# Kernel optimization log

Hardware: AMD Instinct MI355X
Metric: run time of the kernel (lower is better)

The kernel has to match this reference:

```python
import jax, jax.numpy as jnp
import numpy as np

B, S, T = 16, 256, 2048
V, D, H, L, FF, NM = 3000, 512, 8, 6, 2048, 80
DH = D // H


def _make_pe(max_len=5000, d=D):
    pos = np.arange(max_len, dtype=np.float32)[:, None]
    div = np.exp(np.arange(0, d, 2, dtype=np.float32) * (-np.log(10000.0) / d))
    pe = np.zeros((max_len, d), dtype=np.float32)
    pe[:, 0::2] = np.sin(pos * div)
    pe[:, 1::2] = np.cos(pos * div)
    return jnp.asarray(pe[None])  # [1, max_len, D]


def setup_inputs() -> dict:
    key = jax.random.key(0)
    ks = jax.random.split(key, 24)
    f = jnp.float32
    n = lambda k, sh, s=0.02: jax.random.normal(k, sh, f) * s
    return {
        'text_ids': jax.random.randint(ks[0], (B, S), 0, V),
        'text_lengths': jax.random.randint(ks[1], (B,), S // 2, S + 1),
        'mel_targets': jax.random.normal(ks[2], (B, NM, T), f),
        'emb': n(ks[3], (V, D), 0.05),
        'pe': _make_pe(),
        'Wqkv': n(ks[4], (L, D, 3 * D)), 'bqkv': jnp.zeros((L, 3 * D), f),
        'Wo': n(ks[5], (L, D, D)), 'bo': jnp.zeros((L, D), f),
        'ln1_s': jnp.ones((L, D), f), 'ln1_b': jnp.zeros((L, D), f),
        'ln2_s': jnp.ones((L, D), f), 'ln2_b': jnp.zeros((L, D), f),
        'W1': n(ks[6], (L, D, FF)), 'b1': jnp.zeros((L, FF), f),
        'W2': n(ks[7], (L, FF, D)), 'b2': jnp.zeros((L, D), f),
        'mel_W1': n(ks[8], (D, FF)), 'mel_b1': jnp.zeros((FF,), f),
        'mel_W2': n(ks[9], (FF, NM)), 'mel_b2': jnp.zeros((NM,), f),
        'dur_W1': n(ks[10], (D, 256)), 'dur_b1': jnp.zeros((256,), f),
        'dur_W2': n(ks[11], (256, 1)), 'dur_b2': jnp.zeros((1,), f),
    }


def _layer_norm(x, s, b, eps=1e-5):
    m = jnp.mean(x, -1, keepdims=True)
    v = jnp.mean(jnp.square(x - m), -1, keepdims=True)
    return (x - m) * jax.lax.rsqrt(v + eps) * s + b


def _length_regulate(enc, durations, target_len):
    # enc [B,S,D], durations [B,S] -> [B,target_len,D]
    dur = jnp.maximum(jnp.round(durations).astype(jnp.int32), 1)
    cum = jnp.cumsum(dur, axis=1)                              # [B,S] inclusive
    pos = jnp.arange(target_len)                               # [T]
    idx = jnp.sum(pos[None, None, :] >= cum[:, :, None], axis=1)  # [B,T]
    idx = jnp.minimum(idx, enc.shape[1] - 1)
    valid = pos[None, :] < cum[:, -1:]                         # [B,T]
    out = jnp.take_along_axis(enc, idx[..., None], axis=1)
    return out * valid[..., None].astype(enc.dtype)


def reference(text_ids, text_lengths, mel_targets, emb, pe, Wqkv, bqkv, Wo, bo,
              ln1_s, ln1_b, ln2_s, ln2_b, W1, b1, W2, b2,
              mel_W1, mel_b1, mel_W2, mel_b2, dur_W1, dur_b1, dur_W2, dur_b2):
    x = emb[text_ids] + pe[:, :S]                              # [B,S,D]
    pad = jnp.arange(S)[None, :] >= text_lengths[:, None]      # True = padded key
    bias = jnp.where(pad, -1e9, 0.0)[:, None, None, :]         # [B,1,1,S]
    scale = 1.0 / jnp.sqrt(jnp.float32(DH))
    for l in range(L):
        qkv = x @ Wqkv[l] + bqkv[l]
        q, k, v = jnp.split(qkv, 3, axis=-1)
        q = q.reshape(B, S, H, DH).transpose(0, 2, 1, 3)
        k = k.reshape(B, S, H, DH).transpose(0, 2, 1, 3)
        v = v.reshape(B, S, H, DH).transpose(0, 2, 1, 3)
        scores = jnp.einsum('bhqd,bhkd->bhqk', q, k) * scale + bias
        attn = jax.nn.softmax(scores, axis=-1)
        o = jnp.einsum('bhqk,bhkd->bhqd', attn, v)
        o = o.transpose(0, 2, 1, 3).reshape(B, S, D) @ Wo[l] + bo[l]
        x = _layer_norm(x + o, ln1_s[l], ln1_b[l])              # post-LN (torch default)
        ff = jax.nn.relu(x @ W1[l] + b1[l]) @ W2[l] + b2[l]
        x = _layer_norm(x + ff, ln2_s[l], ln2_b[l])
    enc = x
    dur_h = jax.nn.relu(enc @ dur_W1 + dur_b1)
    durations = jax.nn.softplus((dur_h @ dur_W2 + dur_b2).squeeze(-1))  # [B,S]
    target_len = mel_targets.shape[2]
    expanded = _length_regulate(enc, durations, target_len)    # [B,T,D]
    mel = jax.nn.relu(expanded @ mel_W1 + mel_b1) @ mel_W2 + mel_b2
    mel = mel.transpose(0, 2, 1)                               # [B,NM,T]
    return mel, durations, enc
```

## Files before the change

### kernel.cpp

```cpp
#include <hip/hip_runtime.h>
#include <math.h>

#define B_ 16
#define S_ 256
#define T_ 2048
#define D_ 512
#define H_ 8
#define L_ 6
#define FF_ 2048
#define NM_ 80
#define M_ 4096

typedef float floatx4 __attribute__((ext_vector_type(4)));
typedef __bf16 bf16x8 __attribute__((ext_vector_type(8)));

__device__ __forceinline__ float bf2f(unsigned u) {
    return __uint_as_float((u & 0xffffu) << 16);
}
__device__ __forceinline__ unsigned short f2bf(float f) {
    unsigned u = __float_as_uint(f);
    unsigned r = u + 0x7fffu + ((u >> 16) & 1u);
    return (unsigned short)(r >> 16);
}
__device__ __forceinline__ void gload_lds16(const void* g, void* l) {
    __builtin_amdgcn_global_load_lds(
        (const __attribute__((address_space(1))) void*)g,
        (__attribute__((address_space(3))) void*)l, 16, 0, 0);
}

__global__ __launch_bounds__(256) void transpose_bf16(
    const float* __restrict__ src, unsigned short* __restrict__ dst,
    int K, int N)
{
    __shared__ float tile[32][33];
    const int k0 = blockIdx.y * 32, n0 = blockIdx.x * 32;
    src += (size_t)blockIdx.z * K * N;
    dst += (size_t)blockIdx.z * K * N;
    const int tx = threadIdx.x, ty = threadIdx.y;
#pragma unroll
    for (int i = 0; i < 32; i += 8)
        tile[ty + i][tx] = src[(size_t)(k0 + ty + i) * N + n0 + tx];
    __syncthreads();
#pragma unroll
    for (int i = 0; i < 32; i += 8)
        dst[(size_t)(n0 + ty + i) * K + k0 + tx] = f2bf(tile[tx][ty + i]);
}

__global__ __launch_bounds__(256) void transpose_pad_bf16(
    const float* __restrict__ src, unsigned short* __restrict__ dst,
    int K, int Ns)
{
    __shared__ float tile[32][33];
    const int k0 = blockIdx.y * 32, n0 = blockIdx.x * 32;
    const int tx = threadIdx.x, ty = threadIdx.y;
#pragma unroll
    for (int i = 0; i < 32; i += 8) {
        int n = n0 + tx;
        tile[ty + i][tx] = (n < Ns) ? src[(size_t)(k0 + ty + i) * Ns + n] : 0.f;
    }
    __syncthreads();
#pragma unroll
    for (int i = 0; i < 32; i += 8)
        dst[(size_t)(n0 + ty + i) * K + k0 + tx] = f2bf(tile[tx][ty + i]);
}

__global__ __launch_bounds__(128) void embed_bf16(
    const int* __restrict__ ids, const float* __restrict__ emb,
    const float* __restrict__ pe, unsigned short* __restrict__ x)
{
    const int r = blockIdx.x;
    const int c = threadIdx.x * 4;
    const int id = ids[r];
    const int s = r & (S_ - 1);
    float4 e = *(const float4*)(emb + (size_t)id * D_ + c);
    float4 p = *(const float4*)(pe + (size_t)s * D_ + c);
    ushort4 o;
    o.x = f2bf(e.x + p.x); o.y = f2bf(e.y + p.y);
    o.z = f2bf(e.z + p.z); o.w = f2bf(e.w + p.w);
    *(ushort4*)(x + (size_t)r * D_ + c) = o;
}

template<int BM, int BN>
__global__ __launch_bounds__(256) void gemm2(
    const unsigned short* __restrict__ A, const unsigned short* __restrict__ Bt,
    const float* __restrict__ bias, unsigned short* __restrict__ Cb,
    float* __restrict__ Cpart, int N, int klen, int act)
{
    constexpr int NSUB_A = BM / 8;
    constexpr int NSUB_B = BN / 8;
    constexpr int NSUB = NSUB_A + NSUB_B;
    constexpr int NL = NSUB / 4;
    constexpr int BUFSZ = NSUB * 1024;
    constexpr int AOFF = NSUB_A * 1024;
    constexpr int WM = BM / 32, WN = BN / 32;
    __shared__ __attribute__((aligned(16))) char smem[2 * BUFSZ];

    const int tid = threadIdx.x;
    const int wave = tid >> 6, lane = tid & 63;
    const int lm = lane & 15, quad = lane >> 4;
    const int wm = wave >> 1, wn = wave & 1;
    const int m0 = blockIdx.y * BM;
    const int n0 = blockIdx.x * BN;
    const int Kfull = klen * gridDim.z;
    const int kb = blockIdx.z * klen;

    floatx4 acc[WM][WN];
#pragma unroll
    for (int i = 0; i < WM; i++)
#pragma unroll
        for (int j = 0; j < WN; j++) acc[i][j] = (floatx4){0.f, 0.f, 0.f, 0.f};

    const unsigned short* ga[NL];
    int loff[NL];
#pragma unroll
    for (int j = 0; j < NL; j++) {
        int sid = wave * NL + j;
        if (sid < NSUB_A) {
            int mi = sid >> 1, ki = sid & 1;
            ga[j] = A + (size_t)(m0 + mi * 16 + lm) * Kfull + kb + ki * 32 + quad * 8;
            loff[j] = sid * 1024;
        } else {
            int t = sid - NSUB_A;
            int ni = t >> 1, ki = t & 1;
            ga[j] = Bt + (size_t)(n0 + ni * 16 + lm) * Kfull + kb + ki * 32 + quad * 8;
            loff[j] = AOFF + t * 1024;
        }
    }

#pragma unroll
    for (int j = 0; j < NL; j++) gload_lds16(ga[j], smem + loff[j]);

    for (int kt = 0; kt < klen; kt += 64) {
        char* sc = smem + ((kt >> 6) & 1) * BUFSZ;
        if (kt + 64 < klen) {
            char* sn = smem + (((kt >> 6) + 1) & 1) * BUFSZ;
#pragma unroll
            for (int j = 0; j < NL; j++) gload_lds16(ga[j] + kt + 64, sn + loff[j]);
            __builtin_amdgcn_s_waitcnt(0x0F70 | NL);
        } else {
            __builtin_amdgcn_s_waitcnt(0x0F70);
        }
        asm volatile("" ::: "memory");
        __builtin_amdgcn_s_barrier();
        asm volatile("" ::: "memory");

#pragma unroll
        for (int ki = 0; ki < 2; ki++) {
            bf16x8 af[WM], bfr[WN];
#pragma unroll
            for (int i = 0; i < WM; i++)
                af[i] = *(const bf16x8*)(sc + ((((wm * WM + i) * 2 + ki) << 10) + (lane << 4)));
#pragma unroll
            for (int j = 0; j < WN; j++)
                bfr[j] = *(const bf16x8*)(sc + AOFF + ((((wn * WN + j) * 2 + ki) << 10) + (lane << 4)));
#pragma unroll
            for (int i = 0; i < WM; i++)
#pragma unroll
                for (int j = 0; j < WN; j++)
                    acc[i][j] = __builtin_amdgcn_mfma_f32_16x16x32_bf16(
                        af[i], bfr[j], acc[i][j], 0, 0, 0);
        }
        asm volatile("" ::: "memory");
        __builtin_amdgcn_s_barrier();
        asm volatile("" ::: "memory");
    }

    if (gridDim.z == 1) {
#pragma unroll
        for (int mi = 0; mi < WM; mi++) {
            const int rb = m0 + wm * (WM * 16) + mi * 16 + quad * 4;
#pragma unroll
            for (int nj = 0; nj < WN; nj++) {
                const int col = n0 + wn * (WN * 16) + nj * 16 + lm;
                const float bv = bias[col];
#pragma unroll
                for (int r = 0; r < 4; r++) {
                    float o = acc[mi][nj][r] + bv;
                    if (act) o = fmaxf(o, 0.f);
                    Cb[(size_t)(rb + r) * N + col] = f2bf(o);
                }
            }
        }
    } else {
        float* Cp = Cpart + (size_t)blockIdx.z * gridDim.y * BM * N;
#pragma unroll
        for (int mi = 0; mi < WM; mi++) {
            const int rb = m0 + wm * (WM * 16) + mi * 16 + quad * 4;
#pragma unroll
            for (int nj = 0; nj < WN; nj++) {
                const int col = n0 + wn * (WN * 16) + nj * 16 + lm;
#pragma unroll
                for (int r = 0; r < 4; r++)
                    Cp[(size_t)(rb + r) * N + col] = acc[mi][nj][r];
            }
        }
    }
}

__global__ __launch_bounds__(256) void transpose_v(
    const unsigned short* __restrict__ qkv, unsigned short* __restrict__ vt)
{
    __shared__ unsigned short tile[64][74];
    const int tid = threadIdx.x;
    const int bh = blockIdx.y;
    const int b = bh >> 3, h = bh & 7;
    const int s0 = blockIdx.x * 64;
    const int ty = tid >> 3, tx = tid & 7;
#pragma unroll
    for (int i = 0; i < 64; i += 32) {
        uint4 v = *(const uint4*)(qkv + (size_t)(b * 256 + s0 + ty + i) * 1536
                                  + 1024 + h * 64 + tx * 8);
        unsigned short* dstp = &tile[ty + i][tx * 8];
        const unsigned short* sp = (const unsigned short*)&v;
#pragma unroll
        for (int j = 0; j < 8; j++) dstp[j] = sp[j];
    }
    __syncthreads();
#pragma unroll
    for (int i = 0; i < 64; i += 32) {
        int d = ty + i;
        unsigned short tmp[8];
#pragma unroll
        for (int j = 0; j < 8; j++) tmp[j] = tile[tx * 8 + j][d];
        *(uint4*)(vt + (size_t)(bh * 64 + d) * 256 + s0 + tx * 8) = *(uint4*)tmp;
    }
}

__global__ __launch_bounds__(256) void attn_fused(
    const unsigned short* __restrict__ qkv, const unsigned short* __restrict__ vt,
    const int* __restrict__ lens, unsigned short* __restrict__ o)
{
    __shared__ __attribute__((aligned(16))) char smem[32768];
    const int tid = threadIdx.x;
    const int wave = tid >> 6, lane = tid & 63;
    const int lm = lane & 15, quad = lane >> 4;
    const int qt = blockIdx.x;
    const int bh = blockIdx.y;
    const int b = bh >> 3, h = bh & 7;
    const int len = lens[b];
    const unsigned short* Qb = qkv + ((size_t)b * 256 + qt * 64) * 1536 + h * 64;
    const unsigned short* Kb = qkv + (size_t)b * 256 * 1536 + 512 + h * 64;
    const unsigned short* Vt = vt + (size_t)bh * 64 * 256;
    const int rbase = wave * 16;

#pragma unroll
    for (int j = 0; j < 8; j++) {
        int sid = wave * 8 + j;
        int nf = sid >> 1, kf = sid & 1;
        gload_lds16(Kb + (size_t)(nf * 16 + lm) * 1536 + kf * 32 + quad * 8,
                    smem + sid * 1024);
    }
    bf16x8 aq[2];
#pragma unroll
    for (int kf = 0; kf < 2; kf++)
        aq[kf] = *(const bf16x8*)(Qb + (size_t)(rbase + lm) * 1536 + kf * 32 + quad * 8);
    __syncthreads();

    floatx4 accS[16];
#pragma unroll
    for (int nf = 0; nf < 16; nf++) accS[nf] = (floatx4){0.f, 0.f, 0.f, 0.f};

#pragma unroll
    for (int nf = 0; nf < 16; nf++) {
        bf16x8 bk0 = *(const bf16x8*)(smem + (nf * 2 + 0) * 1024 + lane * 16);
        bf16x8 bk1 = *(const bf16x8*)(smem + (nf * 2 + 1) * 1024 + lane * 16);
        accS[nf] = __builtin_amdgcn_mfma_f32_16x16x32_bf16(aq[0], bk0, accS[nf], 0, 0, 0);
        accS[nf] = __builtin_amdgcn_mfma_f32_16x16x32_bf16(aq[1], bk1, accS[nf], 0, 0, 0);
    }

    float lrow[4];
    const float scale = 0.125f;
#pragma unroll
    for (int r = 0; r < 4; r++) {
        float mx = -1e30f;
#pragma unroll
        for (int nf = 0; nf < 16; nf++) {
            float s = accS[nf][r] * scale + ((nf * 16 + lm >= len) ? -1e9f : 0.f);
            accS[nf][r] = s;
            mx = fmaxf(mx, s);
        }
#pragma unroll
        for (int off = 1; off < 16; off <<= 1) mx = fmaxf(mx, __shfl_xor(mx, off, 64));
        float sum = 0.f;
#pragma unroll
        for (int nf = 0; nf < 16; nf++) {
            float e = __expf(accS[nf][r] - mx);
            accS[nf][r] = e;
            sum += e;
        }
#pragma unroll
        for (int off = 1; off < 16; off <<= 1) sum += __shfl_xor(sum, off, 64);
        lrow[r] = sum;
    }

    floatx4 accO[4];
#pragma unroll
    for (int nj = 0; nj < 4; nj++) accO[nj] = (floatx4){0.f, 0.f, 0.f, 0.f};

    unsigned short* sP = (unsigned short*)smem;
#pragma unroll
    for (int half = 0; half < 2; half++) {
        __syncthreads();
#pragma unroll
        for (int nf2 = 0; nf2 < 8; nf2++) {
            int nf = half * 8 + nf2;
            int row = rbase + quad * 4;
            int col = nf2 * 16 + lm;
#pragma unroll
            for (int r = 0; r < 4; r++)
                sP[(row + r) * 136 + col] = f2bf(accS[nf][r]);
        }
        __syncthreads();
#pragma unroll
        for (int ks2 = 0; ks2 < 4; ks2++) {
            bf16x8 ap = *(const bf16x8*)(sP + (rbase + lm) * 136 + ks2 * 32 + quad * 8);
            int ks = half * 4 + ks2;
#pragma unroll
            for (int nj = 0; nj < 4; nj++) {
                bf16x8 bv = *(const bf16x8*)(Vt + (size_t)(nj * 16 + lm) * 256
                                             + ks * 32 + quad * 8);
                accO[nj] = __builtin_amdgcn_mfma_f32_16x16x32_bf16(ap, bv, accO[nj], 0, 0, 0);
            }
        }
    }

    float inv[4];
#pragma unroll
    for (int r = 0; r < 4; r++) inv[r] = 1.f / lrow[r];
    const int grow = b * 256 + qt * 64 + rbase + quad * 4;
#pragma unroll
    for (int nj = 0; nj < 4; nj++) {
        const int gcol = h * 64 + nj * 16 + lm;
#pragma unroll
        for (int r = 0; r < 4; r++)
            o[(size_t)(grow + r) * 512 + gcol] = f2bf(accO[nj][r] * inv[r]);
    }
}

__global__ __launch_bounds__(128) void add_ln_bf16(
    unsigned short* __restrict__ x, const unsigned short* __restrict__ y,
    const float* __restrict__ s, const float* __restrict__ bb)
{
    __shared__ float red[2];
    const int row = blockIdx.x;
    const int tid = threadIdx.x;
    const int c = tid * 4;
    ushort4 xv = *(const ushort4*)(x + (size_t)row * D_ + c);
    ushort4 yv = *(const ushort4*)(y + (size_t)row * D_ + c);
    float h[4];
    h[0] = bf2f(xv.x) + bf2f(yv.x);
    h[1] = bf2f(xv.y) + bf2f(yv.y);
    h[2] = bf2f(xv.z) + bf2f(yv.z);
    h[3] = bf2f(xv.w) + bf2f(yv.w);

    float sum = h[0] + h[1] + h[2] + h[3];
#pragma unroll
    for (int off = 32; off >= 1; off >>= 1) sum += __shfl_xor(sum, off, 64);
    if ((tid & 63) == 0) red[tid >> 6] = sum;
    __syncthreads();
    float mean = (red[0] + red[1]) * (1.f / 512.f);
    __syncthreads();

    float d[4];
    d[0] = h[0] - mean; d[1] = h[1] - mean; d[2] = h[2] - mean; d[3] = h[3] - mean;
    float sq = d[0] * d[0] + d[1] * d[1] + d[2] * d[2] + d[3] * d[3];
#pragma unroll
    for (int off = 32; off >= 1; off >>= 1) sq += __shfl_xor(sq, off, 64);
    if ((tid & 63) == 0) red[tid >> 6] = sq;
    __syncthreads();
    float var = (red[0] + red[1]) * (1.f / 512.f);
    float rs = rsqrtf(var + 1e-5f);

    float4 sv = *(const float4*)(s + c);
    float4 bv = *(const float4*)(bb + c);
    ushort4 ov;
    ov.x = f2bf(d[0] * rs * sv.x + bv.x);
    ov.y = f2bf(d[1] * rs * sv.y + bv.y);
    ov.z = f2bf(d[2] * rs * sv.z + bv.z);
    ov.w = f2bf(d[3] * rs * sv.w + bv.w);
    *(ushort4*)(x + (size_t)row * D_ + c) = ov;
}

__global__ __launch_bounds__(128) void add_ln_part(
    unsigned short* __restrict__ x, const float* __restrict__ p0,
    const float* __restrict__ p1, const float* __restrict__ bias,
    const float* __restrict__ s, const float* __restrict__ bb,
    float* __restrict__ enc_opt)
{
    __shared__ float red[2];
    const int row = blockIdx.x;
    const int tid = threadIdx.x;
    const int c = tid * 4;
    ushort4 xv = *(const ushort4*)(x + (size_t)row * D_ + c);
    float4 a = *(const float4*)(p0 + (size_t)row * D_ + c);
    float4 bq = *(const float4*)(p1 + (size_t)row * D_ + c);
    float4 bi = *(const float4*)(bias + c);
    float h[4];
    h[0] = bf2f(xv.x) + a.x + bq.x + bi.x;
    h[1] = bf2f(xv.y) + a.y + bq.y + bi.y;
    h[2] = bf2f(xv.z) + a.z + bq.z + bi.z;
    h[3] = bf2f(xv.w) + a.w + bq.w + bi.w;

    float sum = h[0] + h[1] + h[2] + h[3];
#pragma unroll
    for (int off = 32; off >= 1; off >>= 1) sum += __shfl_xor(sum, off, 64);
    if ((tid & 63) == 0) red[tid >> 6] = sum;
    __syncthreads();
    float mean = (red[0] + red[1]) * (1.f / 512.f);
    __syncthreads();

    float d[4];
    d[0] = h[0] - mean; d[1] = h[1] - mean; d[2] = h[2] - mean; d[3] = h[3] - mean;
    float sq = d[0] * d[0] + d[1] * d[1] + d[2] * d[2] + d[3] * d[3];
#pragma unroll
    for (int off = 32; off >= 1; off >>= 1) sq += __shfl_xor(sq, off, 64);
    if ((tid & 63) == 0) red[tid >> 6] = sq;
    __syncthreads();
    float var = (red[0] + red[1]) * (1.f / 512.f);
    float rs = rsqrtf(var + 1e-5f);

    float4 sv = *(const float4*)(s + c);
    float4 bv = *(const float4*)(bb + c);
    float o[4];
    o[0] = d[0] * rs * sv.x + bv.x;
    o[1] = d[1] * rs * sv.y + bv.y;
    o[2] = d[2] * rs * sv.z + bv.z;
    o[3] = d[3] * rs * sv.w + bv.w;
    ushort4 ov;
    ov.x = f2bf(o[0]); ov.y = f2bf(o[1]); ov.z = f2bf(o[2]); ov.w = f2bf(o[3]);
    *(ushort4*)(x + (size_t)row * D_ + c) = ov;
    if (enc_opt) {
        float4 e; e.x = o[0]; e.y = o[1]; e.z = o[2]; e.w = o[3];
        *(float4*)(enc_opt + (size_t)row * D_ + c) = e;
    }
}

__global__ __launch_bounds__(256) void dur_head2(
    const float* __restrict__ p0, const float* __restrict__ p1,
    const float* __restrict__ b1, const float* __restrict__ w2,
    const float* __restrict__ b2, float* __restrict__ durout)
{
    const int tid = threadIdx.x;
    const int w = tid >> 6, lane = tid & 63;
    const int r = blockIdx.x * 4 + w;
    float4 a = *(const float4*)(p0 + (size_t)r * 256 + lane * 4);
    float4 bq = *(const float4*)(p1 + (size_t)r * 256 + lane * 4);
    float4 bi = *(const float4*)(b1 + lane * 4);
    float4 wv = *(const float4*)(w2 + lane * 4);
    float h0 = fmaxf(a.x + bq.x + bi.x, 0.f);
    float h1 = fmaxf(a.y + bq.y + bi.y, 0.f);
    float h2 = fmaxf(a.z + bq.z + bi.z, 0.f);
    float h3 = fmaxf(a.w + bq.w + bi.w, 0.f);
    float p = h0 * wv.x + h1 * wv.y + h2 * wv.z + h3 * wv.w;
#pragma unroll
    for (int off = 32; off >= 1; off >>= 1) p += __shfl_xor(p, off, 64);
    if (lane == 0) {
        float v = p + b2[0];
        durout[r] = (v > 20.f) ? v : log1pf(expf(v));
    }
}

__global__ __launch_bounds__(256) void dur_cumsum(
    const float* __restrict__ dur, int* __restrict__ cum)
{
    __shared__ int sc[256];
    const int b = blockIdx.x, s = threadIdx.x;
    int d = (int)rintf(dur[b * 256 + s]);
    if (d < 1) d = 1;
    sc[s] = d;
    __syncthreads();
    for (int off = 1; off < 256; off <<= 1) {
        int v = sc[s];
        int add = (s >= off) ? sc[s - off] : 0;
        __syncthreads();
        sc[s] = v + add;
        __syncthreads();
    }
    cum[b * 256 + s] = sc[s];
}

__global__ __launch_bounds__(256) void mel_c0(
    const float* __restrict__ b1, const float* __restrict__ W2,
    const float* __restrict__ b2, float* __restrict__ c0)
{
    __shared__ float red[4];
    const int c = blockIdx.x;
    const int tid = threadIdx.x;
    float p = 0.f;
    for (int f = tid; f < 2048; f += 256)
        p += fmaxf(b1[f], 0.f) * W2[(size_t)f * 80 + c];
#pragma unroll
    for (int off = 32; off >= 1; off >>= 1) p += __shfl_xor(p, off, 64);
    if ((tid & 63) == 0) red[tid >> 6] = p;
    __syncthreads();
    if (tid == 0) c0[c] = red[0] + red[1] + red[2] + red[3] + b2[c];
}

__global__ __launch_bounds__(256) void mel_gather2(
    const float* __restrict__ mp, const float* __restrict__ b2,
    const float* __restrict__ c0, const int* __restrict__ cum,
    float* __restrict__ mel_out)
{
    __shared__ float rows[256 * 40];
    __shared__ int sc[256];
    __shared__ float s0[40];
    const int tid = threadIdx.x;
    const int b = blockIdx.z;
    const int cc0 = blockIdx.y * 40;
    sc[tid] = cum[b * 256 + tid];
    if (tid < 40) s0[tid] = c0[cc0 + tid];
    const size_t plane = (size_t)M_ * 128;
    for (int idx = tid; idx < 256 * 40; idx += 256) {
        int r = idx / 40, c = idx - r * 40;
        size_t base = ((size_t)b * 256 + r) * 128 + cc0 + c;
        rows[idx] = mp[base] + mp[plane + base] + mp[2 * plane + base]
                  + mp[3 * plane + base] + b2[cc0 + c];
    }
    __syncthreads();
    const int total = sc[255];
    const int t = blockIdx.x * 256 + tid;
    int lo = 0, hi = 256;
    while (lo < hi) {
        int mid = (lo + hi) >> 1;
        if (sc[mid] <= t) lo = mid + 1; else hi = mid;
    }
    int row = lo < 255 ? lo : 255;
    const bool valid = t < total;
    const float* src = valid ? &rows[row * 40] : s0;
    for (int cc = 0; cc < 40; cc++)
        mel_out[((size_t)b * 80 + cc0 + cc) * T_ + t] = src[cc];
}

extern "C" void kernel_launch(void* const* d_in, const int* in_sizes, int n_in,
                              void* d_out, int out_size, void* d_ws, size_t ws_size,
                              hipStream_t stream)
{
    const int*   text_ids     = (const int*)d_in[0];
    const int*   text_lengths = (const int*)d_in[1];
    const float* emb   = (const float*)d_in[3];
    const float* pe    = (const float*)d_in[4];
    const float* Wqkv  = (const float*)d_in[5];
    const float* bqkv  = (const float*)d_in[6];
    const float* Wo    = (const float*)d_in[7];
    const float* bo    = (const float*)d_in[8];
    const float* ln1_s = (const float*)d_in[9];
    const float* ln1_b = (const float*)d_in[10];
    const float* ln2_s = (const float*)d_in[11];
    const float* ln2_b = (const float*)d_in[12];
    const float* W1    = (const float*)d_in[13];
    const float* b1    = (const float*)d_in[14];
    const float* W2    = (const float*)d_in[15];
    const float* b2    = (const float*)d_in[16];
    const float* mel_W1 = (const float*)d_in[17];
    const float* mel_b1 = (const float*)d_in[18];
    const float* mel_W2 = (const float*)d_in[19];
    const float* mel_b2 = (const float*)d_in[20];
    const float* dur_W1 = (const float*)d_in[21];
    const float* dur_b1 = (const float*)d_in[22];
    const float* dur_W2 = (const float*)d_in[23];
    const float* dur_b2 = (const float*)d_in[24];

    float* out = (float*)d_out;
    float* mel_out = out;
    float* dur_out = out + (size_t)B_ * NM_ * T_;
    float* enc_out = dur_out + (size_t)B_ * S_;

    typedef unsigned short u16;
    char* w = (char*)d_ws;
    u16* Wqkv_t  = (u16*)w;                   w += (size_t)L_ * 1536 * 512 * 2;
    u16* Wo_t    = (u16*)w;                   w += (size_t)L_ * 512 * 512 * 2;
    u16* W1_t    = (u16*)w;                   w += (size_t)L_ * 2048 * 512 * 2;
    u16* W2_t    = (u16*)w;                   w += (size_t)L_ * 512 * 2048 * 2;
    u16* melW1_t = (u16*)w;                   w += (size_t)2048 * 512 * 2;
    u16* melW2_t = (u16*)w;                   w += (size_t)128 * 2048 * 2;
    u16* durW1_t = (u16*)w;                   w += (size_t)256 * 512 * 2;
    u16* x_bf    = (u16*)w;                   w += (size_t)M_ * 512 * 2;
    u16* qkv_bf  = (u16*)w;                   w += (size_t)M_ * 1536 * 2;
    u16* ao_bf   = (u16*)w;                   w += (size_t)M_ * 512 * 2;
    u16* y_bf    = (u16*)w;                   w += (size_t)M_ * 512 * 2;
    char* big    = w;                         w += (size_t)16777216;
    float* c0    = (float*)w;                 w += 512;
    int*   cum   = (int*)w;                   w += (size_t)M_ * 4;

    u16* ffh     = (u16*)big;
    u16* melh    = (u16*)big;
    u16* vt      = (u16*)(big + 12582912);

    float* part2 = (float*)qkv_bf;
    float* dpart = (float*)qkv_bf;
    float* mpart = (float*)(qkv_bf + (size_t)M_ * 512);

    transpose_bf16<<<dim3(48, 16, 6), dim3(32, 8), 0, stream>>>(Wqkv, Wqkv_t, 512, 1536);
    transpose_bf16<<<dim3(16, 16, 6), dim3(32, 8), 0, stream>>>(Wo, Wo_t, 512, 512);
    transpose_bf16<<<dim3(64, 16, 6), dim3(32, 8), 0, stream>>>(W1, W1_t, 512, 2048);
    transpose_bf16<<<dim3(16, 64, 6), dim3(32, 8), 0, stream>>>(W2, W2_t, 2048, 512);
    transpose_bf16<<<dim3(64, 16, 1), dim3(32, 8), 0, stream>>>(mel_W1, melW1_t, 512, 2048);
    transpose_pad_bf16<<<dim3(4, 64), dim3(32, 8), 0, stream>>>(mel_W2, melW2_t, 2048, 80);
    transpose_bf16<<<dim3(8, 16, 1), dim3(32, 8), 0, stream>>>(dur_W1, durW1_t, 512, 256);

    embed_bf16<<<M_, 128, 0, stream>>>(text_ids, emb, pe, x_bf);

    for (int l = 0; l < L_; l++) {
        gemm2<64, 128><<<dim3(12, 64), 256, 0, stream>>>(
            x_bf, Wqkv_t + (size_t)l * 1536 * 512, bqkv + (size_t)l * 1536,
            qkv_bf, nullptr, 1536, 512, 0);
        transpose_v<<<dim3(4, 128), 256, 0, stream>>>(qkv_bf, vt);
        attn_fused<<<dim3(4, 128), 256, 0, stream>>>(qkv_bf, vt, text_lengths, ao_bf);
        gemm2<64, 64><<<dim3(8, 64), 256, 0, stream>>>(
            ao_bf, Wo_t + (size_t)l * 512 * 512, bo + (size_t)l * 512,
            y_bf, nullptr, 512, 512, 0);
        add_ln_bf16<<<M_, 128, 0, stream>>>(
            x_bf, y_bf, ln1_s + (size_t)l * D_, ln1_b + (size_t)l * D_);
        gemm2<64, 128><<<dim3(16, 64), 256, 0, stream>>>(
            x_bf, W1_t + (size_t)l * 2048 * 512, b1 + (size_t)l * 2048,
            ffh, nullptr, 2048, 512, 1);
        gemm2<64, 64><<<dim3(8, 64, 2), 256, 0, stream>>>(
            ffh, W2_t + (size_t)l * 512 * 2048, nullptr,
            nullptr, part2, 512, 1024, 0);
        add_ln_part<<<M_, 128, 0, stream>>>(
            x_bf, part2, part2 + (size_t)M_ * 512, b2 + (size_t)l * 512,
            ln2_s + (size_t)l * D_, ln2_b + (size_t)l * D_,
            (l == L_ - 1) ? enc_out : nullptr);
    }

    gemm2<64, 64><<<dim3(4, 64, 2), 256, 0, stream>>>(
        x_bf, durW1_t, nullptr, nullptr, dpart, 256, 256, 0);
    dur_head2<<<M_ / 4, 256, 0, stream>>>(
        dpart, dpart + (size_t)M_ * 256, dur_b1, dur_W2, dur_b2, dur_out);
    dur_cumsum<<<B_, 256, 0, stream>>>(dur_out, cum);

    gemm2<64, 128><<<dim3(16, 64), 256, 0, stream>>>(
        x_bf, melW1_t, mel_b1, melh, nullptr, 2048, 512, 1);
    gemm2<64, 128><<<dim3(1, 64, 4), 256, 0, stream>>>(
        melh, melW2_t, nullptr, nullptr, mpart, 128, 512, 0);
    mel_c0<<<NM_, 256, 0, stream>>>(mel_b1, mel_W2, mel_b2, c0);
    mel_gather2<<<dim3(T_ / 256, 2, B_), 256, 0, stream>>>(mpart, mel_b2, c0, cum, mel_out);
}
```

Baseline: 993.8 us.

## Fuse V transpose into QKV GEMM epilogue and enlarge GEMM and attention tiles

The QKV GEMM now writes the V block transposed through shared memory straight into the vt buffer, which removes the separate transpose_v kernel and its extra read of qkv. Every GEMM moves to 128-row M tiles, and the attention kernel handles 128 queries per block with two MFMA row groups per wave. Together these cut launches and redundant K loads, but they halve the block count and raise register pressure.

```diff
diff --git a/kernel.cpp b/kernel.cpp
--- a/kernel.cpp
+++ b/kernel.cpp
@@ -84,7 +84,8 @@
 __global__ __launch_bounds__(256) void gemm2(
     const unsigned short* __restrict__ A, const unsigned short* __restrict__ Bt,
     const float* __restrict__ bias, unsigned short* __restrict__ Cb,
-    float* __restrict__ Cpart, int N, int klen, int act)
+    float* __restrict__ Cpart, unsigned short* __restrict__ vtp,
+    int N, int klen, int act)
 {
     constexpr int NSUB_A = BM / 8;
     constexpr int NSUB_B = BN / 8;
@@ -165,6 +166,40 @@
         asm volatile("" ::: "memory");
     }
 
+    if constexpr (BM == 128 && BN == 128) {
+        if (vtp != nullptr && n0 >= 1024) {
+            unsigned short* sT = (unsigned short*)smem;
+#pragma unroll
+            for (int mi = 0; mi < WM; mi++) {
+                const int rl = wm * 64 + mi * 16 + quad * 4;
+#pragma unroll
+                for (int nj = 0; nj < WN; nj++) {
+                    const int cl = wn * 64 + nj * 16 + lm;
+                    const float bv = bias[n0 + cl];
+                    ushort4 t4;
+                    t4.x = f2bf(acc[mi][nj][0] + bv);
+                    t4.y = f2bf(acc[mi][nj][1] + bv);
+                    t4.z = f2bf(acc[mi][nj][2] + bv);
+                    t4.w = f2bf(acc[mi][nj][3] + bv);
+                    *(ushort4*)(sT + cl * 136 + rl) = t4;
+                }
+            }
+            __syncthreads();
+            const int b = m0 >> 8;
+            const int s0 = m0 & 255;
+            const int h0 = (n0 - 1024) >> 6;
+#pragma unroll
+            for (int i = 0; i < 8; i++) {
+                int idx = i * 256 + tid;
+                int d = idx >> 4, c = idx & 15;
+                uint4 v = *(const uint4*)(sT + d * 136 + c * 8);
+                int bh = b * 8 + h0 + (d >> 6);
+                *(uint4*)(vtp + ((size_t)bh * 64 + (d & 63)) * 256 + s0 + c * 8) = v;
+            }
+            return;
+        }
+    }
+
     if (gridDim.z == 1) {
 #pragma unroll
         for (int mi = 0; mi < WM; mi++) {
@@ -197,40 +232,11 @@
     }
 }
 
-__global__ __launch_bounds__(256) void transpose_v(
-    const unsigned short* __restrict__ qkv, unsigned short* __restrict__ vt)
-{
-    __shared__ unsigned short tile[64][74];
-    const int tid = threadIdx.x;
-    const int bh = blockIdx.y;
-    const int b = bh >> 3, h = bh & 7;
-    const int s0 = blockIdx.x * 64;
-    const int ty = tid >> 3, tx = tid & 7;
-#pragma unroll
-    for (int i = 0; i < 64; i += 32) {
-        uint4 v = *(const uint4*)(qkv + (size_t)(b * 256 + s0 + ty + i) * 1536
-                                  + 1024 + h * 64 + tx * 8);
-        unsigned short* dstp = &tile[ty + i][tx * 8];
-        const unsigned short* sp = (const unsigned short*)&v;
-#pragma unroll
-        for (int j = 0; j < 8; j++) dstp[j] = sp[j];
-    }
-    __syncthreads();
-#pragma unroll
-    for (int i = 0; i < 64; i += 32) {
-        int d = ty + i;
-        unsigned short tmp[8];
-#pragma unroll
-        for (int j = 0; j < 8; j++) tmp[j] = tile[tx * 8 + j][d];
-        *(uint4*)(vt + (size_t)(bh * 64 + d) * 256 + s0 + tx * 8) = *(uint4*)tmp;
-    }
-}
-
 __global__ __launch_bounds__(256) void attn_fused(
     const unsigned short* __restrict__ qkv, const unsigned short* __restrict__ vt,
     const int* __restrict__ lens, unsigned short* __restrict__ o)
 {
-    __shared__ __attribute__((aligned(16))) char smem[32768];
+    __shared__ __attribute__((aligned(16))) char smem[34816];
     const int tid = threadIdx.x;
     const int wave = tid >> 6, lane = tid & 63;
     const int lm = lane & 15, quad = lane >> 4;
@@ -238,10 +244,9 @@
     const int bh = blockIdx.y;
     const int b = bh >> 3, h = bh & 7;
     const int len = lens[b];
-    const unsigned short* Qb = qkv + ((size_t)b * 256 + qt * 64) * 1536 + h * 64;
+    const unsigned short* Qb = qkv + ((size_t)b * 256 + qt * 128) * 1536 + h * 64;
     const unsigned short* Kb = qkv + (size_t)b * 256 * 1536 + 512 + h * 64;
     const unsigned short* Vt = vt + (size_t)bh * 64 * 256;
-    const int rbase = wave * 16;
 
 #pragma unroll
     for (int j = 0; j < 8; j++) {
@@ -250,90 +255,112 @@
         gload_lds16(Kb + (size_t)(nf * 16 + lm) * 1536 + kf * 32 + quad * 8,
                     smem + sid * 1024);
     }
-    bf16x8 aq[2];
-#pragma unroll
-    for (int kf = 0; kf < 2; kf++)
-        aq[kf] = *(const bf16x8*)(Qb + (size_t)(rbase + lm) * 1536 + kf * 32 + quad * 8);
-    __syncthreads();
-
-    floatx4 accS[16];
-#pragma unroll
-    for (int nf = 0; nf < 16; nf++) accS[nf] = (floatx4){0.f, 0.f, 0.f, 0.f};
+    bf16x8 aq[2][2];
+#pragma unroll
+    for (int mi = 0; mi < 2; mi++)
+#pragma unroll
+        for (int kf = 0; kf < 2; kf++)
+            aq[mi][kf] = *(const bf16x8*)(Qb + (size_t)(wave * 32 + mi * 16 + lm) * 1536
+                                          + kf * 32 + quad * 8);
+    __syncthreads();
+
+    floatx4 accS[2][16];
+#pragma unroll
+    for (int mi = 0; mi < 2; mi++)
+#pragma unroll
+        for (int nf = 0; nf < 16; nf++) accS[mi][nf] = (floatx4){0.f, 0.f, 0.f, 0.f};
 
 #pragma unroll
     for (int nf = 0; nf < 16; nf++) {
         bf16x8 bk0 = *(const bf16x8*)(smem + (nf * 2 + 0) * 1024 + lane * 16);
         bf16x8 bk1 = *(const bf16x8*)(smem + (nf * 2 + 1) * 1024 + lane * 16);
-        accS[nf] = __builtin_amdgcn_mfma_f32_16x16x32_bf16(aq[0], bk0, accS[nf], 0, 0, 0);
-        accS[nf] = __builtin_amdgcn_mfma_f32_16x16x32_bf16(aq[1], bk1, accS[nf], 0, 0, 0);
-    }
-
-    float lrow[4];
+        accS[0][nf] = __builtin_amdgcn_mfma_f32_16x16x32_bf16(aq[0][0], bk0, accS[0][nf], 0, 0, 0);
+        accS[0][nf] = __builtin_amdgcn_mfma_f32_16x16x32_bf16(aq[0][1], bk1, accS[0][nf], 0, 0, 0);
+        accS[1][nf] = __builtin_amdgcn_mfma_f32_16x16x32_bf16(aq[1][0], bk0, accS[1][nf], 0, 0, 0);
+        accS[1][nf] = __builtin_amdgcn_mfma_f32_16x16x32_bf16(aq[1][1], bk1, accS[1][nf], 0, 0, 0);
+    }
+
+    float lrow[2][4];
     const float scale = 0.125f;
 #pragma unroll
-    for (int r = 0; r < 4; r++) {
-        float mx = -1e30f;
-#pragma unroll
-        for (int nf = 0; nf < 16; nf++) {
-            float s = accS[nf][r] * scale + ((nf * 16 + lm >= len) ? -1e9f : 0.f);
-            accS[nf][r] = s;
-            mx = fmaxf(mx, s);
-        }
-#pragma unroll
-        for (int off = 1; off < 16; off <<= 1) mx = fmaxf(mx, __shfl_xor(mx, off, 64));
-        float sum = 0.f;
-#pragma unroll
-        for (int nf = 0; nf < 16; nf++) {
-            float e = __expf(accS[nf][r] - mx);
-            accS[nf][r] = e;
-            sum += e;
-        }
-#pragma unroll
-        for (int off = 1; off < 16; off <<= 1) sum += __shfl_xor(sum, off, 64);
-        lrow[r] = sum;
-    }
-
-    floatx4 accO[4];
-#pragma unroll
-    for (int nj = 0; nj < 4; nj++) accO[nj] = (floatx4){0.f, 0.f, 0.f, 0.f};
+    for (int mi = 0; mi < 2; mi++)
+#pragma unroll
+        for (int r = 0; r < 4; r++) {
+            float mx = -1e30f;
+#pragma unroll
+            for (int nf = 0; nf < 16; nf++) {
+                float s = accS[mi][nf][r] * scale + ((nf * 16 + lm >= len) ? -1e9f : 0.f);
+                accS[mi][nf][r] = s;
+                mx = fmaxf(mx, s);
+            }
+#pragma unroll
+            for (int off = 1; off < 16; off <<= 1) mx = fmaxf(mx, __shfl_xor(mx, off, 64));
+            float sum = 0.f;
+#pragma unroll
+            for (int nf = 0; nf < 16; nf++) {
+                float e = __expf(accS[mi][nf][r] - mx);
+                accS[mi][nf][r] = e;
+                sum += e;
+            }
+#pragma unroll
+            for (int off = 1; off < 16; off <<= 1) sum += __shfl_xor(sum, off, 64);
+            lrow[mi][r] = sum;
+        }
+
+    floatx4 accO[2][4];
+#pragma unroll
+    for (int mi = 0; mi < 2; mi++)
+#pragma unroll
+        for (int nj = 0; nj < 4; nj++) accO[mi][nj] = (floatx4){0.f, 0.f, 0.f, 0.f};
 
     unsigned short* sP = (unsigned short*)smem;
+    const int rbase = wave * 32;
 #pragma unroll
     for (int half = 0; half < 2; half++) {
         __syncthreads();
 #pragma unroll
-        for (int nf2 = 0; nf2 < 8; nf2++) {
-            int nf = half * 8 + nf2;
-            int row = rbase + quad * 4;
-            int col = nf2 * 16 + lm;
-#pragma unroll
-            for (int r = 0; r < 4; r++)
-                sP[(row + r) * 136 + col] = f2bf(accS[nf][r]);
-        }
+        for (int mi = 0; mi < 2; mi++)
+#pragma unroll
+            for (int nf2 = 0; nf2 < 8; nf2++) {
+                int nf = half * 8 + nf2;
+                int row = rbase + mi * 16 + quad * 4;
+                int col = nf2 * 16 + lm;
+#pragma unroll
+                for (int r = 0; r < 4; r++)
+                    sP[(row + r) * 136 + col] = f2bf(accS[mi][nf][r]);
+            }
         __syncthreads();
 #pragma unroll
         for (int ks2 = 0; ks2 < 4; ks2++) {
-            bf16x8 ap = *(const bf16x8*)(sP + (rbase + lm) * 136 + ks2 * 32 + quad * 8);
+            bf16x8 ap[2];
+#pragma unroll
+            for (int mi = 0; mi < 2; mi++)
+                ap[mi] = *(const bf16x8*)(sP + (rbase + mi * 16 + lm) * 136
+                                          + ks2 * 32 + quad * 8);
             int ks = half * 4 + ks2;
 #pragma unroll
             for (int nj = 0; nj < 4; nj++) {
                 bf16x8 bv = *(const bf16x8*)(Vt + (size_t)(nj * 16 + lm) * 256
                                              + ks * 32 + quad * 8);
-                accO[nj] = __builtin_amdgcn_mfma_f32_16x16x32_bf16(ap, bv, accO[nj], 0, 0, 0);
-            }
-        }
-    }
-
-    float inv[4];
-#pragma unroll
-    for (int r = 0; r < 4; r++) inv[r] = 1.f / lrow[r];
-    const int grow = b * 256 + qt * 64 + rbase + quad * 4;
-#pragma unroll
-    for (int nj = 0; nj < 4; nj++) {
-        const int gcol = h * 64 + nj * 16 + lm;
-#pragma unroll
-        for (int r = 0; r < 4; r++)
-            o[(size_t)(grow + r) * 512 + gcol] = f2bf(accO[nj][r] * inv[r]);
+                accO[0][nj] = __builtin_amdgcn_mfma_f32_16x16x32_bf16(ap[0], bv, accO[0][nj], 0, 0, 0);
+                accO[1][nj] = __builtin_amdgcn_mfma_f32_16x16x32_bf16(ap[1], bv, accO[1][nj], 0, 0, 0);
+            }
+        }
+    }
+
+#pragma unroll
+    for (int mi = 0; mi < 2; mi++) {
+        float inv[4];
+#pragma unroll
+        for (int r = 0; r < 4; r++) inv[r] = 1.f / lrow[mi][r];
+        const int grow = b * 256 + qt * 128 + rbase + mi * 16 + quad * 4;
+#pragma unroll
+        for (int nj = 0; nj < 4; nj++) {
+            const int gcol = h * 64 + nj * 16 + lm;
+#pragma unroll
+            for (int r = 0; r < 4; r++)
+                o[(size_t)(grow + r) * 512 + gcol] = f2bf(accO[mi][nj][r] * inv[r]);
+        }
     }
 }
 
@@ -601,38 +628,37 @@
     embed_bf16<<<M_, 128, 0, stream>>>(text_ids, emb, pe, x_bf);
 
     for (int l = 0; l < L_; l++) {
-        gemm2<64, 128><<<dim3(12, 64), 256, 0, stream>>>(
+        gemm2<128, 128><<<dim3(12, 32), 256, 0, stream>>>(
             x_bf, Wqkv_t + (size_t)l * 1536 * 512, bqkv + (size_t)l * 1536,
-            qkv_bf, nullptr, 1536, 512, 0);
-        transpose_v<<<dim3(4, 128), 256, 0, stream>>>(qkv_bf, vt);
-        attn_fused<<<dim3(4, 128), 256, 0, stream>>>(qkv_bf, vt, text_lengths, ao_bf);
-        gemm2<64, 64><<<dim3(8, 64), 256, 0, stream>>>(
+            qkv_bf, nullptr, vt, 1536, 512, 0);
+        attn_fused<<<dim3(2, 128), 256, 0, stream>>>(qkv_bf, vt, text_lengths, ao_bf);
+        gemm2<128, 64><<<dim3(8, 32), 256, 0, stream>>>(
             ao_bf, Wo_t + (size_t)l * 512 * 512, bo + (size_t)l * 512,
-            y_bf, nullptr, 512, 512, 0);
+            y_bf, nullptr, nullptr, 512, 512, 0);
         add_ln_bf16<<<M_, 128, 0, stream>>>(
             x_bf, y_bf, ln1_s + (size_t)l * D_, ln1_b + (size_t)l * D_);
-        gemm2<64, 128><<<dim3(16, 64), 256, 0, stream>>>(
+        gemm2<128, 128><<<dim3(16, 32), 256, 0, stream>>>(
             x_bf, W1_t + (size_t)l * 2048 * 512, b1 + (size_t)l * 2048,
-            ffh, nullptr, 2048, 512, 1);
-        gemm2<64, 64><<<dim3(8, 64, 2), 256, 0, stream>>>(
+            ffh, nullptr, nullptr, 2048, 512, 1);
+        gemm2<128, 64><<<dim3(8, 32, 2), 256, 0, stream>>>(
             ffh, W2_t + (size_t)l * 512 * 2048, nullptr,
-            nullptr, part2, 512, 1024, 0);
+            nullptr, part2, nullptr, 512, 1024, 0);
         add_ln_part<<<M_, 128, 0, stream>>>(
             x_bf, part2, part2 + (size_t)M_ * 512, b2 + (size_t)l * 512,
             ln2_s + (size_t)l * D_, ln2_b + (size_t)l * D_,
             (l == L_ - 1) ? enc_out : nullptr);
     }
 
-    gemm2<64, 64><<<dim3(4, 64, 2), 256, 0, stream>>>(
-        x_bf, durW1_t, nullptr, nullptr, dpart, 256, 256, 0);
+    gemm2<128, 64><<<dim3(4, 32, 2), 256, 0, stream>>>(
+        x_bf, durW1_t, nullptr, nullptr, dpart, nullptr, 256, 256, 0);
     dur_head2<<<M_ / 4, 256, 0, stream>>>(
         dpart, dpart + (size_t)M_ * 256, dur_b1, dur_W2, dur_b2, dur_out);
     dur_cumsum<<<B_, 256, 0, stream>>>(dur_out, cum);
 
-    gemm2<64, 128><<<dim3(16, 64), 256, 0, stream>>>(
-        x_bf, melW1_t, mel_b1, melh, nullptr, 2048, 512, 1);
-    gemm2<64, 128><<<dim3(1, 64, 4), 256, 0, stream>>>(
-        melh, melW2_t, nullptr, nullptr, mpart, 128, 512, 0);
+    gemm2<128, 128><<<dim3(16, 32), 256, 0, stream>>>(
+        x_bf, melW1_t, mel_b1, melh, nullptr, nullptr, 2048, 512, 1);
+    gemm2<128, 64><<<dim3(2, 32, 4), 256, 0, stream>>>(
+        melh, melW2_t, nullptr, nullptr, mpart, nullptr, 128, 512, 0);
     mel_c0<<<NM_, 256, 0, stream>>>(mel_b1, mel_W2, mel_b2, c0);
     mel_gather2<<<dim3(T_ / 256, 2, B_), 256, 0, stream>>>(mpart, mel_b2, c0, cum, mel_out);
 }
```

Measured after the change: 862.0 us. 13.3% less time.
